# Performance work log

Measured on AMD Instinct MI355X. Metric: run time of the kernel, lower is better.

The kernel has to match this reference:

```python
import jax, jax.numpy as jnp
import numpy as np
from jax import lax

B, S, D = 2, 1024, 1024
N = 16            # mamba state dim
EXPAND = 2
DI = EXPAND * D   # inner dim 2048
K = 4             # depthwise conv kernel
H = 16            # soliton heads
DH = D // H
DT_RANK = D // 16
SOL_DT = 0.1      # soliton integration step


def _ln(x, g, b):
    mu = jnp.mean(x, -1, keepdims=True)
    var = jnp.var(x, -1, keepdims=True)
    return (x - mu) / jnp.sqrt(var + 1e-5) * g + b


def setup_inputs() -> dict:
    key = jax.random.key(0)
    ks = jax.random.split(key, 12)
    def nrm(k, sh, sc=0.02):
        return jax.random.normal(k, sh, jnp.float32) * sc
    return {
        'x': nrm(ks[0], (B, S, D), 1.0),
        'ln1_g': jnp.ones(D), 'ln1_b': jnp.zeros(D),
        'W_in': nrm(ks[1], (D, 2 * DI)), 'b_in': jnp.zeros(2 * DI),
        'conv_w': nrm(ks[2], (DI, K), 0.1), 'conv_b': jnp.zeros(DI),
        'W_xp': nrm(ks[3], (DI, DT_RANK + 2 * N)),
        'W_dt': nrm(ks[4], (DT_RANK, DI), 0.1),
        'b_dt': jnp.full((DI,), -4.6),  # softplus(-4.6) ~ 0.01 init dt
        'A_log': jnp.log(jnp.broadcast_to(jnp.arange(1, N + 1, dtype=jnp.float32), (DI, N))),
        'D_skip': jnp.ones(DI),
        'W_out': nrm(ks[5], (DI, D)), 'b_out': jnp.zeros(D),
        'ln2_g': jnp.ones(D), 'ln2_b': jnp.zeros(D),
        'W_si': nrm(ks[6], (D, D)), 'b_si': jnp.zeros(D),
        'gates': nrm(ks[7], (H, 3), 0.1),   # per-head weights for [sine-Gordon, KdV, Heimburg-Jackson]
        'alpha': nrm(ks[8], (H,), 0.1),     # HJ nonlinearity coefficient
        'W_so': nrm(ks[9], (D, D)), 'b_so': jnp.zeros(D),
    }


def _forward(x, ln1_g, ln1_b, W_in, b_in, conv_w, conv_b, W_xp, W_dt, b_dt,
             A_log, D_skip, W_out, b_out, ln2_g, ln2_b, W_si, b_si,
             gates, alpha, W_so, b_so):
    b, s, d = x.shape
    # ---- Mamba mixer branch ----
    u = _ln(x, ln1_g, ln1_b)
    xz = u @ W_in + b_in                                   # [b,s,2*DI]
    xp, z = jnp.split(xz, 2, axis=-1)                      # [b,s,DI] each
    # causal depthwise conv along sequence
    xt = xp.transpose(0, 2, 1)                             # [b,DI,s]
    yc = lax.conv_general_dilated(xt, conv_w[:, None, :], (1,), [(K - 1, 0)],
                                  feature_group_count=DI,
                                  dimension_numbers=('NCW', 'OIW', 'NCW'))
    xc = jax.nn.silu(yc.transpose(0, 2, 1) + conv_b)       # [b,s,DI]
    dbc = xc @ W_xp
    dtr, Bs, Cs = jnp.split(dbc, [DT_RANK, DT_RANK + N], axis=-1)
    dt = jax.nn.softplus(dtr @ W_dt + b_dt)                # [b,s,DI]
    A = -jnp.exp(A_log)                                    # [DI,N]
    dA = jnp.exp(dt[..., None] * A)                        # [b,s,DI,N]
    dBx = (dt * xc)[..., None] * Bs[:, :, None, :]         # [b,s,DI,N]

    def step(h, inp):
        dA_t, dBx_t, C_t = inp
        h = dA_t * h + dBx_t                               # [b,DI,N]
        y = jnp.einsum('bdn,bn->bd', h, C_t)
        return h, y

    h0 = jnp.zeros((b, DI, N), x.dtype)
    xs = (dA.transpose(1, 0, 2, 3), dBx.transpose(1, 0, 2, 3), Cs.transpose(1, 0, 2))
    _, ys = lax.scan(step, h0, xs)
    y = ys.transpose(1, 0, 2)                              # [b,s,DI]
    y = (y + xc * D_skip) * jax.nn.silu(z)
    x = x + y @ W_out + b_out

    # ---- Soliton interaction branch ----
    v = _ln(x, ln2_g, ln2_b)
    uu = (v @ W_si + b_si).reshape(b, s, H, DH)
    up = jnp.pad(uu, ((0, 0), (2, 2), (0, 0), (0, 0)), mode='edge')
    ux = (up[:, 3:-1] - up[:, 1:-3]) * 0.5                 # central 1st derivative
    uxx = up[:, 3:-1] - 2.0 * uu + up[:, 1:-3]
    uxxx = (up[:, 4:] - 2.0 * up[:, 3:-1] + 2.0 * up[:, 1:-3] - up[:, :-4]) * 0.5
    sg = jnp.sin(uu)                                       # sine-Gordon
    kdv = -6.0 * uu * ux - uxxx                            # KdV
    hj = (1.0 + alpha[None, None, :, None] * uu) * uxx     # Heimburg-Jackson
    du = (gates[None, None, :, 0:1] * sg
          + gates[None, None, :, 1:2] * kdv
          + gates[None, None, :, 2:3] * hj)
    sol = (SOL_DT * du).reshape(b, s, d) @ W_so + b_so
    return x + sol


def reference(x, ln1_g, ln1_b, W_in, b_in, conv_w, conv_b, W_xp, W_dt, b_dt,
              A_log, D_skip, W_out, b_out, ln2_g, ln2_b, W_si, b_si,
              gates, alpha, W_so, b_so):
    return _forward(x, ln1_g, ln1_b, W_in, b_in, conv_w, conv_b, W_xp, W_dt, b_dt,
                    A_log, D_skip, W_out, b_out, ln2_g, ln2_b, W_si, b_si,
                    gates, alpha, W_so, b_so)
```

## Files before the change

kernel.cpp:

```cpp
#include <hip/hip_runtime.h>
#include <hip/hip_bf16.h>
#include <math.h>

typedef unsigned short u16;
typedef unsigned int u32;
typedef __attribute__((ext_vector_type(8))) short short8;
typedef __attribute__((ext_vector_type(4))) float f32x4;

constexpr int CB = 2;
constexpr int CS = 1024;
constexpr int CD = 1024;
constexpr int CDI = 2048;
constexpr int CNC2 = 64;
constexpr int CL2 = 16;

__device__ inline u16 f2bf(float v) {
  __hip_bfloat16 h = __float2bfloat16(v);
  return *reinterpret_cast<u16*>(&h);
}
__device__ inline float bf2f(u16 v) {
  return __uint_as_float(((u32)v) << 16);
}

__device__ inline void gload16(const void* g, void* l) {
  __builtin_amdgcn_global_load_lds((const __attribute__((address_space(1))) void*)g,
                                   (__attribute__((address_space(3))) void*)l, 16, 0, 0);
}

struct TJob { const float* src; u16* dst; int K, N, gx, base; };
struct TJobs { TJob j[6]; };

__global__ __launch_bounds__(256)
void transpose_all_kernel(TJobs jobs) {
  int b = blockIdx.x;
  int ji = 0;
#pragma unroll
  for (int i = 1; i < 6; ++i) if (b >= jobs.j[i].base) ji = i;
  TJob jb = jobs.j[ji];
  int lb = b - jb.base;
  int n0 = (lb % jb.gx) * 32, k0 = (lb / jb.gx) * 32;
  __shared__ float tile[32][33];
  int tx = threadIdx.x & 31, ty = threadIdx.x >> 5;
#pragma unroll
  for (int i = 0; i < 4; ++i) {
    int k = k0 + ty + i * 8, n = n0 + tx;
    tile[ty + i * 8][tx] = (n < jb.N) ? jb.src[(size_t)k * jb.N + n] : 0.f;
  }
  __syncthreads();
#pragma unroll
  for (int i = 0; i < 4; ++i) {
    int n = n0 + ty + i * 8, k = k0 + tx;
    jb.dst[(size_t)n * jb.K + k] = f2bf(tile[tx][ty + i * 8]);
  }
}

__global__ __launch_bounds__(256)
void ln_kernel(const float* __restrict__ x, const float* __restrict__ g,
               const float* __restrict__ bb, u16* __restrict__ outb) {
  int row = blockIdx.x;
  const float4* xr = (const float4*)(x + (size_t)row * CD);
  float4 v = xr[threadIdx.x];
  float s = v.x + v.y + v.z + v.w;
  float ss = v.x * v.x + v.y * v.y + v.z * v.z + v.w * v.w;
#pragma unroll
  for (int o = 1; o < 64; o <<= 1) { s += __shfl_xor(s, o); ss += __shfl_xor(ss, o); }
  __shared__ float sb[4], ssb[4];
  int wid = threadIdx.x >> 6;
  if ((threadIdx.x & 63) == 0) { sb[wid] = s; ssb[wid] = ss; }
  __syncthreads();
  s = sb[0] + sb[1] + sb[2] + sb[3];
  ss = ssb[0] + ssb[1] + ssb[2] + ssb[3];
  float mu = s * (1.f / CD);
  float var = ss * (1.f / CD) - mu * mu;
  float rstd = rsqrtf(var + 1e-5f);
  float4 gv = ((const float4*)g)[threadIdx.x];
  float4 bv = ((const float4*)bb)[threadIdx.x];
  ushort4 o;
  o.x = f2bf((v.x - mu) * rstd * gv.x + bv.x);
  o.y = f2bf((v.y - mu) * rstd * gv.y + bv.y);
  o.z = f2bf((v.z - mu) * rstd * gv.z + bv.z);
  o.w = f2bf((v.w - mu) * rstd * gv.w + bv.w);
  ((ushort4*)(outb + (size_t)row * CD))[threadIdx.x] = o;
}

__global__ __launch_bounds__(256)
void ln_fuse_kernel(const float* __restrict__ x, const u16* __restrict__ S,
                    const float* __restrict__ bo, const float* __restrict__ g,
                    const float* __restrict__ bb, float* __restrict__ out,
                    u16* __restrict__ outb) {
  constexpr size_t SSTR = (size_t)2048 * 1024;
  int row = blockIdx.x;
  float4 xv = ((const float4*)(x + (size_t)row * CD))[threadIdx.x];
  float4 bv0 = ((const float4*)bo)[threadIdx.x];
  float4 v;
  v.x = xv.x + bv0.x; v.y = xv.y + bv0.y; v.z = xv.z + bv0.z; v.w = xv.w + bv0.w;
  size_t base = (size_t)row * CD + threadIdx.x * 4;
#pragma unroll
  for (int z = 0; z < 4; ++z) {
    ushort4 sv = *(const ushort4*)(S + z * SSTR + base);
    v.x += bf2f(sv.x); v.y += bf2f(sv.y); v.z += bf2f(sv.z); v.w += bf2f(sv.w);
  }
  ((float4*)(out + (size_t)row * CD))[threadIdx.x] = v;
  float s = v.x + v.y + v.z + v.w;
  float ss = v.x * v.x + v.y * v.y + v.z * v.z + v.w * v.w;
#pragma unroll
  for (int o = 1; o < 64; o <<= 1) { s += __shfl_xor(s, o); ss += __shfl_xor(ss, o); }
  __shared__ float sb[4], ssb[4];
  int wid = threadIdx.x >> 6;
  if ((threadIdx.x & 63) == 0) { sb[wid] = s; ssb[wid] = ss; }
  __syncthreads();
  s = sb[0] + sb[1] + sb[2] + sb[3];
  ss = ssb[0] + ssb[1] + ssb[2] + ssb[3];
  float mu = s * (1.f / CD);
  float var = ss * (1.f / CD) - mu * mu;
  float rstd = rsqrtf(var + 1e-5f);
  float4 gv = ((const float4*)g)[threadIdx.x];
  float4 bv = ((const float4*)bb)[threadIdx.x];
  ushort4 o;
  o.x = f2bf((v.x - mu) * rstd * gv.x + bv.x);
  o.y = f2bf((v.y - mu) * rstd * gv.y + bv.y);
  o.z = f2bf((v.z - mu) * rstd * gv.z + bv.z);
  o.w = f2bf((v.w - mu) * rstd * gv.w + bv.w);
  ((ushort4*)(outb + (size_t)row * CD))[threadIdx.x] = o;
}

__global__ __launch_bounds__(256)
void add3_kernel(float* __restrict__ out, const u16* __restrict__ S,
                 const float* __restrict__ bias) {
  constexpr size_t SSTR = (size_t)2048 * 1024;
  int idx = blockIdx.x * 256 + threadIdx.x;
  int c4 = idx & 255;
  size_t base = (size_t)idx * 4;
  float4 o = ((const float4*)out)[idx];
  float4 bv = ((const float4*)bias)[c4];
  ushort4 a = *(const ushort4*)(S + base);
  ushort4 b = *(const ushort4*)(S + SSTR + base);
  o.x += bf2f(a.x) + bf2f(b.x) + bv.x;
  o.y += bf2f(a.y) + bf2f(b.y) + bv.y;
  o.z += bf2f(a.z) + bf2f(b.z) + bv.z;
  o.w += bf2f(a.w) + bf2f(b.w) + bv.w;
  ((float4*)out)[idx] = o;
}

template<int BN, int LDA, int LDB>
__global__ __launch_bounds__(256)
void gemm5_kernel(const u16* __restrict__ A, const u16* __restrict__ Bt,
                  const float* __restrict__ bias,
                  const float* __restrict__ resid, int ldr,
                  float* __restrict__ C, int ldc,
                  u16* __restrict__ aux, int auxN,
                  int partial_stride, int Nact, int K, int act) {
  constexpr int WN = BN / 32;
  constexpr int AHALF = 128 * 32;
  constexpr int BHALF = BN * 32;
  __shared__ __align__(16) u16 As[2 * AHALF];
  __shared__ __align__(16) u16 Bs[2 * BHALF];
  const int tid = threadIdx.x, lane = tid & 63, wid = tid >> 6;
  const int wr = wid >> 1, wc = wid & 1;
  int nwg = gridDim.x * gridDim.y;
  int bid = blockIdx.y * gridDim.x + blockIdx.x;
  int swz = (bid & 7) * (nwg >> 3) + (bid >> 3);
  int bx = swz / gridDim.y, by = swz % gridDim.y;
  const int bm = by * 128, bn = bx * BN;
  const int kper = K / gridDim.z;
  const int kbeg = blockIdx.z * kper;
  const int nt = kper / 32;

  int a_src[2], b_src[BN / 64];
#pragma unroll
  for (int j = 0; j < 2; ++j) {
    int c = tid + j * 256;
    int row = c >> 2, kc = (c & 3) ^ ((row + (row >> 2)) & 3);
    a_src[j] = (bm + row) * LDA + kc * 8 + kbeg;
  }
#pragma unroll
  for (int j = 0; j < BN / 64; ++j) {
    int c = tid + j * 256;
    int row = c >> 2, kc = (c & 3) ^ ((row + (row >> 2)) & 3);
    b_src[j] = (bn + row) * LDB + kc * 8 + kbeg;
  }
  int afo[4], bfo[WN];
  const int ch = lane >> 4;
#pragma unroll
  for (int m = 0; m < 4; ++m) {
    int r = wr * 64 + m * 16 + (lane & 15);
    afo[m] = r * 32 + ((ch ^ ((r + (r >> 2)) & 3)) << 3);
  }
#pragma unroll
  for (int n = 0; n < WN; ++n) {
    int r = wc * (BN / 2) + n * 16 + (lane & 15);
    bfo[n] = r * 32 + ((ch ^ ((r + (r >> 2)) & 3)) << 3);
  }
  f32x4 acc[4][WN] = {};

  auto stage = [&](int t, int abuf, int bbuf) {
    int k0 = t * 32;
#pragma unroll
    for (int j = 0; j < 2; ++j)
      gload16(A + a_src[j] + k0, As + abuf + (tid + j * 256) * 8);
#pragma unroll
    for (int j = 0; j < BN / 64; ++j)
      gload16(Bt + b_src[j] + k0, Bs + bbuf + (tid + j * 256) * 8);
  };
  auto compute = [&](int abuf, int bbuf) {
    short8 af[4], bfr[WN];
#pragma unroll
    for (int m = 0; m < 4; ++m) af[m] = *(const short8*)&As[abuf + afo[m]];
#pragma unroll
    for (int n = 0; n < WN; ++n) bfr[n] = *(const short8*)&Bs[bbuf + bfo[n]];
#pragma unroll
    for (int m = 0; m < 4; ++m)
#pragma unroll
      for (int n = 0; n < WN; ++n)
        acc[m][n] = __builtin_amdgcn_mfma_f32_16x16x32_bf16(af[m], bfr[n], acc[m][n], 0, 0, 0);
  };

  stage(0, 0, 0);
  __syncthreads();
  int t = 0;
  while (true) {
    if (t + 1 < nt) stage(t + 1, AHALF, BHALF);
    compute(0, 0);
    __syncthreads();
    if (++t == nt) break;
    if (t + 1 < nt) stage(t + 1, 0, 0);
    compute(AHALF, BHALF);
    __syncthreads();
    if (++t == nt) break;
  }

  const int fr = lane & 15, fq = lane >> 4;
  const int ksegs = gridDim.z;
  u16* Cp = (u16*)C + (size_t)blockIdx.z * partial_stride;
#pragma unroll
  for (int m = 0; m < 4; ++m) {
#pragma unroll
    for (int n = 0; n < WN; ++n) {
#pragma unroll
      for (int j = 0; j < 4; ++j) {
        int row = bm + wr * 64 + m * 16 + fq * 4 + j;
        int col = bn + wc * (BN / 2) + n * 16 + fr;
        if (col < Nact) {
          float v = acc[m][n][j];
          if (ksegs == 1) {
            if (bias) v += bias[col];
            if (resid) v += resid[(size_t)row * ldr + col];
            if (act == 1) v = (v > 20.f) ? v : log1pf(__expf(v));
            if (C) C[(size_t)row * ldc + col] = v;
            if (aux && col < auxN) aux[(size_t)row * auxN + col] = f2bf(v);
          } else if (partial_stride > 0) {
            Cp[(size_t)row * ldc + col] = f2bf(v);
          } else {
            atomicAdd(&C[(size_t)row * ldc + col], v);
          }
        }
      }
    }
  }
}

__global__ __launch_bounds__(256)
void conv_silu_kernel(const u16* __restrict__ xz, const float* __restrict__ w,
                      const float* __restrict__ cb, u16* __restrict__ xcb) {
  int idx = blockIdx.x * 256 + threadIdx.x;
  int d0 = (idx & 255) * 8;
  int t = (idx >> 8) & (CS - 1);
  int b = idx >> 18;
  const u16* base = xz + (size_t)(b * CS) * 4096 + d0;
  float acc[8];
  float4 cb2[2] = { ((const float4*)(cb + d0))[0], ((const float4*)(cb + d0))[1] };
#pragma unroll
  for (int i = 0; i < 8; ++i) acc[i] = ((const float*)cb2)[i];
#pragma unroll
  for (int k = 0; k < 4; ++k) {
    int tt = t - 3 + k;
    if (tt >= 0) {
      short8 v = *(const short8*)(base + (size_t)tt * 4096);
#pragma unroll
      for (int i = 0; i < 8; ++i)
        acc[i] = fmaf(bf2f((u16)v[i]), w[(d0 + i) * 4 + k], acc[i]);
    }
  }
  short8 o;
#pragma unroll
  for (int i = 0; i < 8; ++i) {
    float v = acc[i] * (1.f / (1.f + __expf(-acc[i])));
    o[i] = (short)f2bf(v);
  }
  *(short8*)(xcb + (size_t)(b * CS + t) * CDI + d0) = o;
}

__global__ __launch_bounds__(256)
void dbc_combine_kernel(const u16* __restrict__ parts, float* __restrict__ dbc,
                        u16* __restrict__ dtrb) {
  int idx = blockIdx.x * 256 + threadIdx.x;
  int row = idx / 24, c4 = idx % 24;
  int o = row * 96 + c4 * 4;
  float4 s = make_float4(0.f, 0.f, 0.f, 0.f);
#pragma unroll
  for (int z = 0; z < 16; ++z) {
    ushort4 v = *(const ushort4*)(parts + (size_t)z * (2048 * 96) + o);
    s.x += bf2f(v.x); s.y += bf2f(v.y); s.z += bf2f(v.z); s.w += bf2f(v.w);
  }
  *(float4*)(dbc + o) = s;
  if (c4 < 16) {
    ushort4 b;
    b.x = f2bf(s.x); b.y = f2bf(s.y); b.z = f2bf(s.z); b.w = f2bf(s.w);
    *(ushort4*)(dtrb + row * 64 + c4 * 4) = b;
  }
}

__global__ __launch_bounds__(256)
void scan1_kernel(const u16* __restrict__ dtb, const u16* __restrict__ xcb,
                  const float* __restrict__ dbc, const float* __restrict__ A_log,
                  u16* __restrict__ P, u16* __restrict__ Q) {
  int gid = blockIdx.x * 256 + threadIdx.x;
  int d = gid & (CDI - 1);
  int c = (gid >> 11) & (CNC2 - 1);
  int b = gid >> 17;
  float acoef[16];
#pragma unroll
  for (int j = 0; j < 4; ++j) {
    float4 al = ((const float4*)(A_log + d * 16))[j];
    acoef[j * 4 + 0] = -__expf(al.x);
    acoef[j * 4 + 1] = -__expf(al.y);
    acoef[j * 4 + 2] = -__expf(al.z);
    acoef[j * 4 + 3] = -__expf(al.w);
  }
  float Pv[16], Qv[16];
#pragma unroll
  for (int n = 0; n < 16; ++n) { Pv[n] = 1.f; Qv[n] = 0.f; }
  size_t rowbase = (size_t)b * CS + (size_t)c * CL2;
  for (int i = 0; i < CL2; ++i) {
    size_t r = rowbase + i;
    float dtv = bf2f(dtb[r * CDI + d]);
    float xcv = bf2f(xcb[r * CDI + d]);
    float dx = dtv * xcv;
    const float4* bs4 = (const float4*)(dbc + r * 96 + 64);
    float bs[16];
#pragma unroll
    for (int j = 0; j < 4; ++j) {
      float4 t4 = bs4[j];
      bs[j * 4 + 0] = t4.x; bs[j * 4 + 1] = t4.y; bs[j * 4 + 2] = t4.z; bs[j * 4 + 3] = t4.w;
    }
#pragma unroll
    for (int n = 0; n < 16; ++n) {
      float a = __expf(dtv * acoef[n]);
      Pv[n] *= a;
      Qv[n] = fmaf(a, Qv[n], dx * bs[n]);
    }
  }
  size_t o = (((size_t)b * CNC2 + c) * CDI + d) * 16;
  u16 pb[16], qb[16];
#pragma unroll
  for (int n = 0; n < 16; ++n) { pb[n] = f2bf(Pv[n]); qb[n] = f2bf(Qv[n]); }
#pragma unroll
  for (int j = 0; j < 2; ++j) {
    *(short8*)(P + o + j * 8) = *(short8*)(pb + j * 8);
    *(short8*)(Q + o + j * 8) = *(short8*)(qb + j * 8);
  }
}

__global__ __launch_bounds__(256)
void scan2_kernel(const u16* __restrict__ P, u16* __restrict__ Q) {
  int gid = blockIdx.x * 256 + threadIdx.x;
  int n = gid & 15;
  int d = (gid >> 4) & (CDI - 1);
  int b = gid >> 15;
  int obase = ((b * CNC2) * CDI + d) * 16 + n;
  constexpr int CSTRIDE = CDI * 16;
  float h = 0.f;
  for (int c0 = 0; c0 < CNC2; c0 += 8) {
    float pv[8], qv[8];
#pragma unroll
    for (int i = 0; i < 8; ++i) {
      int o = obase + (c0 + i) * CSTRIDE;
      pv[i] = bf2f(P[o]);
      qv[i] = bf2f(Q[o]);
    }
#pragma unroll
    for (int i = 0; i < 8; ++i) {
      int o = obase + (c0 + i) * CSTRIDE;
      Q[o] = f2bf(h);
      h = fmaf(pv[i], h, qv[i]);
    }
  }
}

__global__ __launch_bounds__(256)
void scan3_kernel(const u16* __restrict__ dtb, const u16* __restrict__ xcb,
                  const float* __restrict__ dbc, const float* __restrict__ A_log,
                  const u16* __restrict__ Q, const u16* __restrict__ xz,
                  const float* __restrict__ Dskip, u16* __restrict__ y2b) {
  int gid = blockIdx.x * 256 + threadIdx.x;
  int d = gid & (CDI - 1);
  int c = (gid >> 11) & (CNC2 - 1);
  int b = gid >> 17;
  float acoef[16];
#pragma unroll
  for (int j = 0; j < 4; ++j) {
    float4 al = ((const float4*)(A_log + d * 16))[j];
    acoef[j * 4 + 0] = -__expf(al.x);
    acoef[j * 4 + 1] = -__expf(al.y);
    acoef[j * 4 + 2] = -__expf(al.z);
    acoef[j * 4 + 3] = -__expf(al.w);
  }
  float h[16];
  size_t o = (((size_t)b * CNC2 + c) * CDI + d) * 16;
#pragma unroll
  for (int j = 0; j < 2; ++j) {
    short8 q8 = *(const short8*)(Q + o + j * 8);
#pragma unroll
    for (int n = 0; n < 8; ++n) h[j * 8 + n] = bf2f((u16)q8[n]);
  }
  float dsk = Dskip[d];
  size_t rowbase = (size_t)b * CS + (size_t)c * CL2;
  for (int i = 0; i < CL2; ++i) {
    size_t r = rowbase + i;
    float dtv = bf2f(dtb[r * CDI + d]);
    float xcv = bf2f(xcb[r * CDI + d]);
    float zv = bf2f(xz[r * 4096 + 2048 + d]);
    float dx = dtv * xcv;
    const float4* bc4 = (const float4*)(dbc + r * 96 + 64);
    float bs[16], cs[16];
#pragma unroll
    for (int j = 0; j < 4; ++j) {
      float4 t4 = bc4[j];
      bs[j * 4 + 0] = t4.x; bs[j * 4 + 1] = t4.y; bs[j * 4 + 2] = t4.z; bs[j * 4 + 3] = t4.w;
      float4 u4 = bc4[4 + j];
      cs[j * 4 + 0] = u4.x; cs[j * 4 + 1] = u4.y; cs[j * 4 + 2] = u4.z; cs[j * 4 + 3] = u4.w;
    }
    float y = 0.f;
#pragma unroll
    for (int n = 0; n < 16; ++n) {
      float a = __expf(dtv * acoef[n]);
      h[n] = fmaf(a, h[n], dx * bs[n]);
      y = fmaf(h[n], cs[n], y);
    }
    float sz = zv * (1.f / (1.f + __expf(-zv)));
    y2b[r * CDI + d] = f2bf((y + xcv * dsk) * sz);
  }
}

__global__ __launch_bounds__(256)
void soliton_kernel(const u16* __restrict__ S, const float* __restrict__ bsi,
                    const float* __restrict__ gates, const float* __restrict__ alpha,
                    u16* __restrict__ sol) {
  constexpr size_t SSTR = (size_t)2048 * 1024;
  int idx = blockIdx.x * 256 + threadIdx.x;
  int d = idx & (CD - 1);
  int t = (idx >> 10) & (CS - 1);
  int b = idx >> 20;
  int h = d >> 6;
  size_t base = (size_t)b * CS * CD + d;
  int tm2 = max(t - 2, 0), tm1 = max(t - 1, 0);
  int tp1 = min(t + 1, CS - 1), tp2 = min(t + 2, CS - 1);
  auto val = [&](int tt) {
    size_t off = base + (size_t)tt * CD;
    return bf2f(S[off]) + bf2f(S[SSTR + off]);
  };
  float um2 = val(tm2);
  float um1 = val(tm1);
  float u0r = val(t);
  float up1 = val(tp1);
  float up2 = val(tp2);
  float u0 = u0r + bsi[d];
  float ux   = (up1 - um1) * 0.5f;
  float uxx  = up1 - 2.f * u0r + um1;
  float uxxx = (up2 - 2.f * up1 + 2.f * um1 - um2) * 0.5f;
  float sg = sinf(u0);
  float kdv = -6.f * u0 * ux - uxxx;
  float hj = (1.f + alpha[h] * u0) * uxx;
  float du = gates[h * 3 + 0] * sg + gates[h * 3 + 1] * kdv + gates[h * 3 + 2] * hj;
  sol[idx] = f2bf(0.1f * du);
}

extern "C" void kernel_launch(void* const* d_in, const int* in_sizes, int n_in,
                              void* d_out, int out_size, void* d_ws, size_t ws_size,
                              hipStream_t stream) {
  const float* x      = (const float*)d_in[0];
  const float* ln1_g  = (const float*)d_in[1];
  const float* ln1_b  = (const float*)d_in[2];
  const float* W_in   = (const float*)d_in[3];
  const float* b_in   = (const float*)d_in[4];
  const float* conv_w = (const float*)d_in[5];
  const float* conv_b = (const float*)d_in[6];
  const float* W_xp   = (const float*)d_in[7];
  const float* W_dt   = (const float*)d_in[8];
  const float* b_dt   = (const float*)d_in[9];
  const float* A_log  = (const float*)d_in[10];
  const float* D_skip = (const float*)d_in[11];
  const float* W_out  = (const float*)d_in[12];
  const float* b_out  = (const float*)d_in[13];
  const float* ln2_g  = (const float*)d_in[14];
  const float* ln2_b  = (const float*)d_in[15];
  const float* W_si   = (const float*)d_in[16];
  const float* b_si   = (const float*)d_in[17];
  const float* gates  = (const float*)d_in[18];
  const float* alpha  = (const float*)d_in[19];
  const float* W_so   = (const float*)d_in[20];
  const float* b_so   = (const float*)d_in[21];
  float* out = (float*)d_out;

  float* ws = (float*)d_ws;
  size_t off = 0;
  auto alloc = [&](size_t nwords) { float* p = ws + off; off += nwords; return p; };
  const size_t BS = (size_t)CB * CS;
  const size_t M1 = 1024 * 1024;

  u16* Wt_in  = (u16*)alloc(2 * M1);
  u16* Wt_xp  = (u16*)alloc(128 * 1024);
  u16* Wt_dt  = (u16*)alloc(64 * 1024);
  u16* Wt_out = (u16*)alloc(M1);
  u16* Wt_si  = (u16*)alloc(M1 / 2);
  u16* Wt_so  = (u16*)alloc(M1 / 2);
  u16* u_bf   = (u16*)alloc(M1);
  u16* sol_bf = u_bf;
  u16* xz_bf  = (u16*)alloc(4 * M1);
  u16* dt_bf  = (u16*)alloc(2 * M1);
  u16* xc_bf  = (u16*)alloc(2 * M1);
  float* dbc  = alloc(BS * 96);
  u16* dtr_bf = (u16*)alloc(64 * 1024);
  float* Pb_f = alloc(2 * M1);
  float* Qb_f = alloc(2 * M1);
  u16* Pb = (u16*)Pb_f;
  u16* Qb = (u16*)Qb_f;
  u16* Slab = (u16*)Pb_f;
  u16* y2_bf  = (u16*)alloc(2 * M1);

  dim3 blk(256);
  const int PSTRIDE = (int)(BS * CD);
  const int DBC_STRIDE = 2048 * 96;

  {
    TJobs jobs;
    int base = 0;
    auto mk = [&](const float* s, u16* dst, int K, int N, int Npad) {
      int gx = Npad / 32, gy = K / 32;
      TJob j{s, dst, K, N, gx, base};
      base += gx * gy;
      return j;
    };
    jobs.j[0] = mk(W_in, Wt_in, 1024, 4096, 4096);
    jobs.j[1] = mk(W_xp, Wt_xp, 2048, 96, 128);
    jobs.j[2] = mk(W_dt, Wt_dt, 64, 2048, 2048);
    jobs.j[3] = mk(W_out, Wt_out, 2048, 1024, 1024);
    jobs.j[4] = mk(W_si, Wt_si, 1024, 1024, 1024);
    jobs.j[5] = mk(W_so, Wt_so, 1024, 1024, 1024);
    transpose_all_kernel<<<base, blk, 0, stream>>>(jobs);
  }

  ln_kernel<<<BS, blk, 0, stream>>>(x, ln1_g, ln1_b, u_bf);
  gemm5_kernel<64, 1024, 1024><<<dim3(64, 16), blk, 0, stream>>>(
      u_bf, Wt_in, b_in, nullptr, 0, nullptr, 0, xz_bf, 4096, 0, 4096, 1024, 0);
  conv_silu_kernel<<<(BS * CDI) / (256 * 8), blk, 0, stream>>>(xz_bf, conv_w, conv_b, xc_bf);
  gemm5_kernel<64, 2048, 2048><<<dim3(2, 16, 16), blk, 0, stream>>>(
      xc_bf, Wt_xp, nullptr, nullptr, 0, (float*)Slab, 96, nullptr, 0, DBC_STRIDE, 96, 2048, 0);
  dbc_combine_kernel<<<(2048 * 24) / 256, blk, 0, stream>>>(Slab, dbc, dtr_bf);
  gemm5_kernel<64, 64, 64><<<dim3(32, 16), blk, 0, stream>>>(
      dtr_bf, Wt_dt, b_dt, nullptr, 0, nullptr, 0, dt_bf, 2048, 0, 2048, 64, 1);
  scan1_kernel<<<(CB * CNC2 * CDI) / 256, blk, 0, stream>>>(dt_bf, xc_bf, dbc, A_log, Pb, Qb);
  scan2_kernel<<<(CB * CDI * 16) / 256, blk, 0, stream>>>(Pb, Qb);
  scan3_kernel<<<(CB * CNC2 * CDI) / 256, blk, 0, stream>>>(dt_bf, xc_bf, dbc, A_log, Qb, xz_bf, D_skip, y2_bf);
  gemm5_kernel<64, 2048, 2048><<<dim3(16, 16, 4), blk, 0, stream>>>(
      y2_bf, Wt_out, nullptr, nullptr, 0, (float*)Slab, CD, nullptr, 0, PSTRIDE, 1024, 2048, 0);
  ln_fuse_kernel<<<BS, blk, 0, stream>>>(x, Slab, b_out, ln2_g, ln2_b, out, u_bf);
  gemm5_kernel<64, 1024, 1024><<<dim3(16, 16, 2), blk, 0, stream>>>(
      u_bf, Wt_si, nullptr, nullptr, 0, (float*)Slab, CD, nullptr, 0, PSTRIDE, 1024, 1024, 0);
  soliton_kernel<<<(BS * CD) / 256, blk, 0, stream>>>(Slab, b_si, gates, alpha, sol_bf);
  gemm5_kernel<64, 1024, 1024><<<dim3(16, 16, 2), blk, 0, stream>>>(
      sol_bf, Wt_so, nullptr, nullptr, 0, (float*)Slab, CD, nullptr, 0, PSTRIDE, 1024, 1024, 0);
  add3_kernel<<<(BS * CD) / (256 * 4), blk, 0, stream>>>(out, Slab, b_so);
}
```

Baseline: 246.1 us.

## Split-K the input projection and fold LN1 into the transpose launch

The first layer norm now runs as extra blocks inside the weight-transpose kernel, which removes one launch. The W_in GEMM is split into two K-halves that write bf16 partial slabs, which doubles the grid from 1024 to 2048 blocks. The conv and scan3 kernels sum the two partials and add b_in when they read. This trades better GEMM occupancy and one fewer launch for twice the xz storage and extra reads, plus a small loss of precision from summing two bf16 partials.

Result: slower. 258.6 us (+5.1%).

```diff
diff --git a/kernel.cpp b/kernel.cpp
--- a/kernel.cpp
+++ b/kernel.cpp
@@ -31,8 +31,37 @@
 struct TJobs { TJob j[6]; };
 
 __global__ __launch_bounds__(256)
-void transpose_all_kernel(TJobs jobs) {
+void transpose_ln_kernel(TJobs jobs, int lnbase, const float* __restrict__ x,
+                         const float* __restrict__ g, const float* __restrict__ bb,
+                         u16* __restrict__ outb) {
   int b = blockIdx.x;
+  if (b >= lnbase) {
+    int row = b - lnbase;
+    const float4* xr = (const float4*)(x + (size_t)row * CD);
+    float4 v = xr[threadIdx.x];
+    float s = v.x + v.y + v.z + v.w;
+    float ss = v.x * v.x + v.y * v.y + v.z * v.z + v.w * v.w;
+#pragma unroll
+    for (int o = 1; o < 64; o <<= 1) { s += __shfl_xor(s, o); ss += __shfl_xor(ss, o); }
+    __shared__ float sb[4], ssb[4];
+    int wid = threadIdx.x >> 6;
+    if ((threadIdx.x & 63) == 0) { sb[wid] = s; ssb[wid] = ss; }
+    __syncthreads();
+    s = sb[0] + sb[1] + sb[2] + sb[3];
+    ss = ssb[0] + ssb[1] + ssb[2] + ssb[3];
+    float mu = s * (1.f / CD);
+    float var = ss * (1.f / CD) - mu * mu;
+    float rstd = rsqrtf(var + 1e-5f);
+    float4 gv = ((const float4*)g)[threadIdx.x];
+    float4 bv = ((const float4*)bb)[threadIdx.x];
+    ushort4 o;
+    o.x = f2bf((v.x - mu) * rstd * gv.x + bv.x);
+    o.y = f2bf((v.y - mu) * rstd * gv.y + bv.y);
+    o.z = f2bf((v.z - mu) * rstd * gv.z + bv.z);
+    o.w = f2bf((v.w - mu) * rstd * gv.w + bv.w);
+    ((ushort4*)(outb + (size_t)row * CD))[threadIdx.x] = o;
+    return;
+  }
   int ji = 0;
 #pragma unroll
   for (int i = 1; i < 6; ++i) if (b >= jobs.j[i].base) ji = i;
@@ -54,34 +83,6 @@
   }
 }
 
-__global__ __launch_bounds__(256)
-void ln_kernel(const float* __restrict__ x, const float* __restrict__ g,
-               const float* __restrict__ bb, u16* __restrict__ outb) {
-  int row = blockIdx.x;
-  const float4* xr = (const float4*)(x + (size_t)row * CD);
-  float4 v = xr[threadIdx.x];
-  float s = v.x + v.y + v.z + v.w;
-  float ss = v.x * v.x + v.y * v.y + v.z * v.z + v.w * v.w;
-#pragma unroll
-  for (int o = 1; o < 64; o <<= 1) { s += __shfl_xor(s, o); ss += __shfl_xor(ss, o); }
-  __shared__ float sb[4], ssb[4];
-  int wid = threadIdx.x >> 6;
-  if ((threadIdx.x & 63) == 0) { sb[wid] = s; ssb[wid] = ss; }
-  __syncthreads();
-  s = sb[0] + sb[1] + sb[2] + sb[3];
-  ss = ssb[0] + ssb[1] + ssb[2] + ssb[3];
-  float mu = s * (1.f / CD);
-  float var = ss * (1.f / CD) - mu * mu;
-  float rstd = rsqrtf(var + 1e-5f);
-  float4 gv = ((const float4*)g)[threadIdx.x];
-  float4 bv = ((const float4*)bb)[threadIdx.x];
-  ushort4 o;
-  o.x = f2bf((v.x - mu) * rstd * gv.x + bv.x);
-  o.y = f2bf((v.y - mu) * rstd * gv.y + bv.y);
-  o.z = f2bf((v.z - mu) * rstd * gv.z + bv.z);
-  o.w = f2bf((v.w - mu) * rstd * gv.w + bv.w);
-  ((ushort4*)(outb + (size_t)row * CD))[threadIdx.x] = o;
-}
 
 __global__ __launch_bounds__(256)
 void ln_fuse_kernel(const float* __restrict__ x, const u16* __restrict__ S,
@@ -260,25 +261,31 @@
 }
 
 __global__ __launch_bounds__(256)
-void conv_silu_kernel(const u16* __restrict__ xz, const float* __restrict__ w,
-                      const float* __restrict__ cb, u16* __restrict__ xcb) {
+void conv_silu_kernel(const u16* __restrict__ xz, const float* __restrict__ bin,
+                      const float* __restrict__ w, const float* __restrict__ cb,
+                      u16* __restrict__ xcb) {
+  constexpr size_t XSTR = (size_t)2048 * 4096;
   int idx = blockIdx.x * 256 + threadIdx.x;
   int d0 = (idx & 255) * 8;
   int t = (idx >> 8) & (CS - 1);
   int b = idx >> 18;
   const u16* base = xz + (size_t)(b * CS) * 4096 + d0;
-  float acc[8];
+  float acc[8], bi[8];
   float4 cb2[2] = { ((const float4*)(cb + d0))[0], ((const float4*)(cb + d0))[1] };
-#pragma unroll
-  for (int i = 0; i < 8; ++i) acc[i] = ((const float*)cb2)[i];
+  float4 bi2[2] = { ((const float4*)(bin + d0))[0], ((const float4*)(bin + d0))[1] };
+#pragma unroll
+  for (int i = 0; i < 8; ++i) { acc[i] = ((const float*)cb2)[i]; bi[i] = ((const float*)bi2)[i]; }
 #pragma unroll
   for (int k = 0; k < 4; ++k) {
     int tt = t - 3 + k;
     if (tt >= 0) {
-      short8 v = *(const short8*)(base + (size_t)tt * 4096);
-#pragma unroll
-      for (int i = 0; i < 8; ++i)
-        acc[i] = fmaf(bf2f((u16)v[i]), w[(d0 + i) * 4 + k], acc[i]);
+      short8 v0 = *(const short8*)(base + (size_t)tt * 4096);
+      short8 v1 = *(const short8*)(base + XSTR + (size_t)tt * 4096);
+#pragma unroll
+      for (int i = 0; i < 8; ++i) {
+        float xpv = bf2f((u16)v0[i]) + bf2f((u16)v1[i]) + bi[i];
+        acc[i] = fmaf(xpv, w[(d0 + i) * 4 + k], acc[i]);
+      }
     }
   }
   short8 o;
@@ -391,7 +398,9 @@
 void scan3_kernel(const u16* __restrict__ dtb, const u16* __restrict__ xcb,
                   const float* __restrict__ dbc, const float* __restrict__ A_log,
                   const u16* __restrict__ Q, const u16* __restrict__ xz,
-                  const float* __restrict__ Dskip, u16* __restrict__ y2b) {
+                  const float* __restrict__ bin, const float* __restrict__ Dskip,
+                  u16* __restrict__ y2b) {
+  constexpr size_t XSTR = (size_t)2048 * 4096;
   int gid = blockIdx.x * 256 + threadIdx.x;
   int d = gid & (CDI - 1);
   int c = (gid >> 11) & (CNC2 - 1);
@@ -414,12 +423,14 @@
     for (int n = 0; n < 8; ++n) h[j * 8 + n] = bf2f((u16)q8[n]);
   }
   float dsk = Dskip[d];
+  float bz = bin[2048 + d];
   size_t rowbase = (size_t)b * CS + (size_t)c * CL2;
   for (int i = 0; i < CL2; ++i) {
     size_t r = rowbase + i;
     float dtv = bf2f(dtb[r * CDI + d]);
     float xcv = bf2f(xcb[r * CDI + d]);
-    float zv = bf2f(xz[r * 4096 + 2048 + d]);
+    size_t zo = r * 4096 + 2048 + d;
+    float zv = bf2f(xz[zo]) + bf2f(xz[XSTR + zo]) + bz;
     float dx = dtv * xcv;
     const float4* bc4 = (const float4*)(dbc + r * 96 + 64);
     float bs[16], cs[16];
@@ -516,7 +527,7 @@
   u16* Wt_so  = (u16*)alloc(M1 / 2);
   u16* u_bf   = (u16*)alloc(M1);
   u16* sol_bf = u_bf;
-  u16* xz_bf  = (u16*)alloc(4 * M1);
+  u16* xz_bf  = (u16*)alloc(8 * M1);
   u16* dt_bf  = (u16*)alloc(2 * M1);
   u16* xc_bf  = (u16*)alloc(2 * M1);
   float* dbc  = alloc(BS * 96);
@@ -529,7 +540,8 @@
   u16* y2_bf  = (u16*)alloc(2 * M1);
 
   dim3 blk(256);
-  const int PSTRIDE = (int)(BS * CD);
+  const int PSTRIDE  = (int)(BS * CD);
+  const int XZSTRIDE = (int)(BS * 4096);
   const int DBC_STRIDE = 2048 * 96;
 
   {
@@ -547,13 +559,12 @@
     jobs.j[3] = mk(W_out, Wt_out, 2048, 1024, 1024);
     jobs.j[4] = mk(W_si, Wt_si, 1024, 1024, 1024);
     jobs.j[5] = mk(W_so, Wt_so, 1024, 1024, 1024);
-    transpose_all_kernel<<<base, blk, 0, stream>>>(jobs);
-  }
-
-  ln_kernel<<<BS, blk, 0, stream>>>(x, ln1_g, ln1_b, u_bf);
-  gemm5_kernel<64, 1024, 1024><<<dim3(64, 16), blk, 0, stream>>>(
-      u_bf, Wt_in, b_in, nullptr, 0, nullptr, 0, xz_bf, 4096, 0, 4096, 1024, 0);
-  conv_silu_kernel<<<(BS * CDI) / (256 * 8), blk, 0, stream>>>(xz_bf, conv_w, conv_b, xc_bf);
+    transpose_ln_kernel<<<base + (int)BS, blk, 0, stream>>>(jobs, base, x, ln1_g, ln1_b, u_bf);
+  }
+
+  gemm5_kernel<64, 1024, 1024><<<dim3(64, 16, 2), blk, 0, stream>>>(
+      u_bf, Wt_in, nullptr, nullptr, 0, (float*)xz_bf, 4096, nullptr, 0, XZSTRIDE, 4096, 1024, 0);
+  conv_silu_kernel<<<(BS * CDI) / (256 * 8), blk, 0, stream>>>(xz_bf, b_in, conv_w, conv_b, xc_bf);
   gemm5_kernel<64, 2048, 2048><<<dim3(2, 16, 16), blk, 0, stream>>>(
       xc_bf, Wt_xp, nullptr, nullptr, 0, (float*)Slab, 96, nullptr, 0, DBC_STRIDE, 96, 2048, 0);
   dbc_combine_kernel<<<(2048 * 24) / 256, blk, 0, stream>>>(Slab, dbc, dtr_bf);
@@ -561,7 +572,7 @@
       dtr_bf, Wt_dt, b_dt, nullptr, 0, nullptr, 0, dt_bf, 2048, 0, 2048, 64, 1);
   scan1_kernel<<<(CB * CNC2 * CDI) / 256, blk, 0, stream>>>(dt_bf, xc_bf, dbc, A_log, Pb, Qb);
   scan2_kernel<<<(CB * CDI * 16) / 256, blk, 0, stream>>>(Pb, Qb);
-  scan3_kernel<<<(CB * CNC2 * CDI) / 256, blk, 0, stream>>>(dt_bf, xc_bf, dbc, A_log, Qb, xz_bf, D_skip, y2_bf);
+  scan3_kernel<<<(CB * CNC2 * CDI) / 256, blk, 0, stream>>>(dt_bf, xc_bf, dbc, A_log, Qb, xz_bf, b_in, D_skip, y2_bf);
   gemm5_kernel<64, 2048, 2048><<<dim3(16, 16, 4), blk, 0, stream>>>(
       y2_bf, Wt_out, nullptr, nullptr, 0, (float*)Slab, CD, nullptr, 0, PSTRIDE, 1024, 2048, 0);
   ln_fuse_kernel<<<BS, blk, 0, stream>>>(x, Slab, b_out, ln2_g, ln2_b, out, u_bf);
```
